# Kernel tuning notes

Measured on AMD Instinct MI355X. Metric: run time of the kernel, lower is better.

The kernel has to match this reference:

```python
import jax, jax.numpy as jnp
import numpy as np

N_EMBD = 2048
N_HEAD = 32
N_KV_HEAD = 8
HEAD_DIM = N_EMBD // N_HEAD  # 64
N_REP = N_HEAD // N_KV_HEAD  # 4
B, T = 2, 2048


def setup_inputs() -> dict:
    key = jax.random.key(0)
    ks = jax.random.split(key, 9)
    s = 1.0 / np.sqrt(N_EMBD)
    kv_dim = N_KV_HEAD * HEAD_DIM
    return {
        "x": jax.random.normal(ks[0], (B, T, N_EMBD), dtype=jnp.float32),
        "Wq": jax.random.normal(ks[1], (N_EMBD, N_EMBD), dtype=jnp.float32) * s,
        "bq": jax.random.normal(ks[2], (N_EMBD,), dtype=jnp.float32) * 0.01,
        "Wk": jax.random.normal(ks[3], (N_EMBD, kv_dim), dtype=jnp.float32) * s,
        "bk": jax.random.normal(ks[4], (kv_dim,), dtype=jnp.float32) * 0.01,
        "Wv": jax.random.normal(ks[5], (N_EMBD, kv_dim), dtype=jnp.float32) * s,
        "bv": jax.random.normal(ks[6], (kv_dim,), dtype=jnp.float32) * 0.01,
        "Wo": jax.random.normal(ks[7], (N_EMBD, N_EMBD), dtype=jnp.float32) * s,
        "bo": jax.random.normal(ks[8], (N_EMBD,), dtype=jnp.float32) * 0.01,
    }


def reference(x, Wq, bq, Wk, bk, Wv, bv, Wo, bo):
    Bsz, Tlen, C = x.shape
    # projections
    q = (x @ Wq + bq).reshape(Bsz, Tlen, N_HEAD, HEAD_DIM).transpose(0, 2, 1, 3)   # [B,H,T,d]
    k = (x @ Wk + bk).reshape(Bsz, Tlen, N_KV_HEAD, HEAD_DIM).transpose(0, 2, 1, 3)  # [B,Hkv,T,d]
    v = (x @ Wv + bv).reshape(Bsz, Tlen, N_KV_HEAD, HEAD_DIM).transpose(0, 2, 1, 3)
    # repeat_interleave KV heads to match query heads
    k = jnp.repeat(k, N_REP, axis=1)  # [B,H,T,d]
    v = jnp.repeat(v, N_REP, axis=1)
    # causal SDPA
    scale = 1.0 / jnp.sqrt(jnp.asarray(HEAD_DIM, dtype=x.dtype))
    scores = jnp.einsum('bhqd,bhkd->bhqk', q, k) * scale  # [B,H,T,T]
    causal = jnp.tril(jnp.ones((Tlen, Tlen), dtype=bool))
    scores = jnp.where(causal, scores, jnp.asarray(-jnp.inf, dtype=scores.dtype))
    attn = jax.nn.softmax(scores, axis=-1)
    y = jnp.einsum('bhqk,bhkd->bhqd', attn, v)  # [B,H,T,d]
    y = y.transpose(0, 2, 1, 3).reshape(Bsz, Tlen, C)
    return y @ Wo + bo
```

## Files before the change

### kernel.cpp

```cpp
#include <hip/hip_runtime.h>
#include <hip/hip_bf16.h>

#define B_SZ   2
#define T_SEQ  2048
#define C_EMB  2048
#define KV_DIM 512

typedef __bf16 bf16x8 __attribute__((ext_vector_type(8)));
typedef __bf16 bf16x4 __attribute__((ext_vector_type(4)));
typedef float  f32x4  __attribute__((ext_vector_type(4)));
typedef float  f32x16 __attribute__((ext_vector_type(16)));
typedef unsigned int u32;

typedef __attribute__((address_space(1))) const unsigned int gu32;
typedef __attribute__((address_space(3))) unsigned int lu32;
__device__ __forceinline__ void gload16(const void* g, void* l) {
  __builtin_amdgcn_global_load_lds((gu32*)g, (lu32*)l, 16, 0, 0);
}

__global__ __launch_bounds__(256) void cast_f32_bf16(const float* __restrict__ in,
                                                     __bf16* __restrict__ out, int n8) {
  int i = blockIdx.x * 256 + threadIdx.x;
  if (i < n8) {
    const float4* p = (const float4*)(in + (size_t)i * 8);
    float4 a = p[0], b = p[1];
    bf16x8 o;
    o[0] = (__bf16)a.x; o[1] = (__bf16)a.y; o[2] = (__bf16)a.z; o[3] = (__bf16)a.w;
    o[4] = (__bf16)b.x; o[5] = (__bf16)b.y; o[6] = (__bf16)b.z; o[7] = (__bf16)b.w;
    *(bf16x8*)(out + (size_t)i * 8) = o;
  }
}

__global__ __launch_bounds__(256) void transpose_cast_kernel(const float* __restrict__ in,
                                                             __bf16* __restrict__ out,
                                                             int R, int C) {
  __shared__ float tile[64][65];
  int c0 = blockIdx.x * 64, r0 = blockIdx.y * 64;
  int tid = threadIdx.x;
#pragma unroll
  for (int i = 0; i < 4; i++) {
    int idx = tid + i * 256;
    int row = idx >> 4;
    int c4  = (idx & 15) * 4;
    float4 v = *(const float4*)&in[(size_t)(r0 + row) * C + c0 + c4];
    tile[row][c4 + 0] = v.x; tile[row][c4 + 1] = v.y;
    tile[row][c4 + 2] = v.z; tile[row][c4 + 3] = v.w;
  }
  __syncthreads();
#pragma unroll
  for (int i = 0; i < 4; i++) {
    int idx = tid + i * 256;
    int col = idx >> 4;
    int r4  = (idx & 15) * 4;
    bf16x4 o;
    o[0] = (__bf16)tile[r4 + 0][col];
    o[1] = (__bf16)tile[r4 + 1][col];
    o[2] = (__bf16)tile[r4 + 2][col];
    o[3] = (__bf16)tile[r4 + 3][col];
    *(bf16x4*)&out[(size_t)(c0 + col) * R + r0 + r4] = o;
  }
}

__global__ __launch_bounds__(256) void concat_bias(const float* __restrict__ bq,
                                                   const float* __restrict__ bk,
                                                   const float* __restrict__ bv,
                                                   float* __restrict__ bcat) {
  int i = blockIdx.x * 256 + threadIdx.x;
  if (i < 3072) {
    float v = (i < 2048) ? bq[i] : (i < 2560 ? bk[i - 2048] : bv[i - 2560]);
    bcat[i] = v;
  }
}

template <int MODE>
__global__ __launch_bounds__(256) void gemm_bt(const __bf16* __restrict__ A,
                                               const __bf16* __restrict__ Bt,
                                               const float* __restrict__ bias,
                                               void* __restrict__ out0,
                                               __bf16* __restrict__ outK,
                                               __bf16* __restrict__ outV,
                                               int M, int N, int K) {
  __shared__ __bf16 As[128 * 32];
  __shared__ __bf16 Bs[128 * 32];
  int tid  = threadIdx.x;
  int lane = tid & 63, wave = tid >> 6;
  int wr = wave >> 1, wc = wave & 1;
  int la = lane & 15, kg = lane >> 4;
  int m0 = blockIdx.x * 128, n0 = blockIdx.y * 128;

  f32x4 acc[4][4];
#pragma unroll
  for (int i = 0; i < 4; i++)
#pragma unroll
    for (int j = 0; j < 4; j++)
#pragma unroll
      for (int r = 0; r < 4; r++) acc[i][j][r] = 0.f;

  int s0 = tid, s1 = tid + 256;
  const __bf16* ga0 = A  + (size_t)(m0 + (s0 >> 2)) * K + (s0 & 3) * 8;
  const __bf16* ga1 = A  + (size_t)(m0 + (s1 >> 2)) * K + (s1 & 3) * 8;
  const __bf16* gb0 = Bt + (size_t)(n0 + (s0 >> 2)) * K + (s0 & 3) * 8;
  const __bf16* gb1 = Bt + (size_t)(n0 + (s1 >> 2)) * K + (s1 & 3) * 8;
  __bf16* lA0 = As + (size_t)(0 * 256 + wave * 64) * 8;
  __bf16* lA1 = As + (size_t)(1 * 256 + wave * 64) * 8;
  __bf16* lB0 = Bs + (size_t)(0 * 256 + wave * 64) * 8;
  __bf16* lB1 = Bs + (size_t)(1 * 256 + wave * 64) * 8;

  for (int k0 = 0; k0 < K; k0 += 32) {
    gload16(ga0 + k0, lA0);
    gload16(ga1 + k0, lA1);
    gload16(gb0 + k0, lB0);
    gload16(gb1 + k0, lB1);
    __syncthreads();
    bf16x8 af[4], bfr[4];
#pragma unroll
    for (int i = 0; i < 4; i++) af[i]  = *(const bf16x8*)&As[(size_t)(wr * 64 + i * 16 + la) * 32 + kg * 8];
#pragma unroll
    for (int j = 0; j < 4; j++) bfr[j] = *(const bf16x8*)&Bs[(size_t)(wc * 64 + j * 16 + la) * 32 + kg * 8];
#pragma unroll
    for (int i = 0; i < 4; i++)
#pragma unroll
      for (int j = 0; j < 4; j++)
        acc[i][j] = __builtin_amdgcn_mfma_f32_16x16x32_bf16(af[i], bfr[j], acc[i][j], 0, 0, 0);
    __syncthreads();
  }

#pragma unroll
  for (int i = 0; i < 4; i++) {
    int rowb = m0 + wr * 64 + i * 16 + kg * 4;
#pragma unroll
    for (int j = 0; j < 4; j++) {
      int col = n0 + wc * 64 + j * 16 + la;
      float bv = bias[col];
#pragma unroll
      for (int r = 0; r < 4; r++) {
        float v = acc[i][j][r] + bv;
        if (MODE == 2) {
          ((float*)out0)[(size_t)(rowb + r) * N + col] = v;
        } else {
          if (n0 < 2048)      ((__bf16*)out0)[(size_t)(rowb + r) * 2048 + col] = (__bf16)v;
          else if (n0 < 2560) outK[(size_t)(rowb + r) * 512 + (col - 2048)] = (__bf16)v;
          else                outV[(size_t)(col - 2560) * M + rowb + r] = (__bf16)v;
        }
      }
    }
  }
}

__global__ __launch_bounds__(128) void attn_kernel(const __bf16* __restrict__ Q,
                                                   const __bf16* __restrict__ K,
                                                   const __bf16* __restrict__ Vt,
                                                   __bf16* __restrict__ Y) {
  __shared__ __bf16 Ylds[2][32][72];
  const int M = B_SZ * T_SEQ;
  int tid = threadIdx.x;
  int wv = tid >> 6, l = tid & 63;
  int qcol = l & 31, hh = l >> 5;
  int g = blockIdx.x;
  int w = (g & 7) * 256 + (g >> 3);
  int bh = w >> 5;
  int qt = 31 - (w & 31);
  int b = bh >> 5, hq = bh & 31, kvh = hq >> 2;
  int q0w = qt * 64 + wv * 32;

  const __bf16* qrow = Q + (size_t)(b * T_SEQ + q0w + qcol) * C_EMB + hq * 64;
  bf16x8 qf[4];
#pragma unroll
  for (int c = 0; c < 4; c++) qf[c] = *(const bf16x8*)(qrow + c * 16 + hh * 8);

  f32x16 acc0, acc1;
#pragma unroll
  for (int r = 0; r < 16; r++) { acc0[r] = 0.f; acc1[r] = 0.f; }
  float m_run = -1e30f, l_run = 0.f;
  const float SC = 0.125f * 1.44269504f;

  const __bf16* kbase = K + (size_t)(b * T_SEQ) * KV_DIM + kvh * 64;
  const __bf16* v0 = Vt + (size_t)(kvh * 64 + qcol) * M + (size_t)b * T_SEQ;
  const __bf16* v1 = v0 + (size_t)32 * M;

  for (int kb = 0; kb <= q0w; kb += 32) {
    f32x16 s;
#pragma unroll
    for (int r = 0; r < 16; r++) s[r] = 0.f;
    const __bf16* krow = kbase + (size_t)(kb + qcol) * KV_DIM;
#pragma unroll
    for (int c = 0; c < 4; c++) {
      bf16x8 kf = *(const bf16x8*)(krow + c * 16 + hh * 8);
      s = __builtin_amdgcn_mfma_f32_32x32x16_bf16(kf, qf[c], s, 0, 0, 0);
    }
    if (kb == q0w) {
#pragma unroll
      for (int r = 0; r < 16; r++) {
        int kr = (r & 3) + 8 * (r >> 2) + 4 * hh;
        s[r] = (kr <= qcol) ? s[r] : -1e30f;
      }
    }
    float mloc = s[0];
#pragma unroll
    for (int r = 1; r < 16; r++) mloc = fmaxf(mloc, s[r]);
    mloc = fmaxf(mloc, __shfl_xor(mloc, 32, 64));
    if (__any(mloc > m_run + 33.0f)) {
      float mnew = fmaxf(m_run, mloc);
      float corr = exp2f((m_run - mnew) * SC);
      l_run *= corr;
#pragma unroll
      for (int r = 0; r < 16; r++) { acc0[r] *= corr; acc1[r] *= corr; }
      m_run = mnew;
    }
    float p[16]; float ps = 0.f;
#pragma unroll
    for (int r = 0; r < 16; r++) { p[r] = exp2f((s[r] - m_run) * SC); ps += p[r]; }
    ps += __shfl_xor(ps, 32, 64);
    l_run += ps;
    u32 P[8];
#pragma unroll
    for (int j = 0; j < 8; j++) {
      union { __bf16 b2[2]; u32 u; } pk;
      pk.b2[0] = (__bf16)p[2 * j]; pk.b2[1] = (__bf16)p[2 * j + 1];
      P[j] = pk.u;
    }
    u32 xP[8];
#pragma unroll
    for (int j = 0; j < 8; j++) xP[j] = (u32)__shfl_xor((int)P[j], 32, 64);
    union { u32 u[4]; bf16x8 v; } w0u, w1u;
    w0u.u[0] = hh ? xP[2] : P[0];
    w0u.u[1] = hh ? xP[3] : P[1];
    w0u.u[2] = hh ? P[2]  : xP[0];
    w0u.u[3] = hh ? P[3]  : xP[1];
    w1u.u[0] = hh ? xP[6] : P[4];
    w1u.u[1] = hh ? xP[7] : P[5];
    w1u.u[2] = hh ? P[6]  : xP[4];
    w1u.u[3] = hh ? P[7]  : xP[5];
    const __bf16* vr0 = v0 + kb;
    const __bf16* vr1 = v1 + kb;
    bf16x8 vf00 = *(const bf16x8*)(vr0 + hh * 8);
    bf16x8 vf01 = *(const bf16x8*)(vr0 + 16 + hh * 8);
    bf16x8 vf10 = *(const bf16x8*)(vr1 + hh * 8);
    bf16x8 vf11 = *(const bf16x8*)(vr1 + 16 + hh * 8);
    acc0 = __builtin_amdgcn_mfma_f32_32x32x16_bf16(vf00, w0u.v, acc0, 0, 0, 0);
    acc0 = __builtin_amdgcn_mfma_f32_32x32x16_bf16(vf01, w1u.v, acc0, 0, 0, 0);
    acc1 = __builtin_amdgcn_mfma_f32_32x32x16_bf16(vf10, w0u.v, acc1, 0, 0, 0);
    acc1 = __builtin_amdgcn_mfma_f32_32x32x16_bf16(vf11, w1u.v, acc1, 0, 0, 0);
  }

  float inv = 1.0f / l_run;
  __bf16 (*slab)[72] = Ylds[wv];
#pragma unroll
  for (int r = 0; r < 16; r++) {
    int drow = (r & 3) + 8 * (r >> 2) + 4 * hh;
    slab[qcol][drow]      = (__bf16)(acc0[r] * inv);
    slab[qcol][32 + drow] = (__bf16)(acc1[r] * inv);
  }
  __syncthreads();
  __bf16* yrow = Y + (size_t)(b * T_SEQ + q0w + qcol) * C_EMB + hq * 64 + hh * 32;
#pragma unroll
  for (int c = 0; c < 4; c++)
    *(bf16x8*)(yrow + c * 8) = *(const bf16x8*)&slab[qcol][hh * 32 + c * 8];
}

extern "C" void kernel_launch(void* const* d_in, const int* in_sizes, int n_in,
                              void* d_out, int out_size, void* d_ws, size_t ws_size,
                              hipStream_t stream) {
  const float* x  = (const float*)d_in[0];
  const float* Wq = (const float*)d_in[1];
  const float* bq = (const float*)d_in[2];
  const float* Wk = (const float*)d_in[3];
  const float* bk = (const float*)d_in[4];
  const float* Wv = (const float*)d_in[5];
  const float* bv = (const float*)d_in[6];
  const float* Wo = (const float*)d_in[7];
  const float* bo = (const float*)d_in[8];
  float* out = (float*)d_out;

  const int M = B_SZ * T_SEQ;

  char* w = (char*)d_ws;
  __bf16* xb   = (__bf16*)w; w += (size_t)M * C_EMB * 2;
  __bf16* Wall = (__bf16*)w; w += (size_t)3072 * C_EMB * 2;
  __bf16* Wot  = (__bf16*)w; w += (size_t)C_EMB * C_EMB * 2;
  float*  bcat = (float*)w;  w += (size_t)3072 * 4;
  __bf16* qb   = (__bf16*)w; w += (size_t)M * C_EMB * 2;
  __bf16* kbf  = (__bf16*)w; w += (size_t)M * KV_DIM * 2;
  __bf16* vbt  = (__bf16*)w; w += (size_t)KV_DIM * M * 2;
  __bf16* yb   = (__bf16*)w; w += (size_t)M * C_EMB * 2;

  cast_f32_bf16<<<(M * C_EMB / 8 + 255) / 256, 256, 0, stream>>>(x, xb, M * C_EMB / 8);

  transpose_cast_kernel<<<dim3(C_EMB / 64, C_EMB / 64), 256, 0, stream>>>(Wq, Wall, C_EMB, C_EMB);
  transpose_cast_kernel<<<dim3(KV_DIM / 64, C_EMB / 64), 256, 0, stream>>>(Wk, Wall + (size_t)2048 * C_EMB, C_EMB, KV_DIM);
  transpose_cast_kernel<<<dim3(KV_DIM / 64, C_EMB / 64), 256, 0, stream>>>(Wv, Wall + (size_t)2560 * C_EMB, C_EMB, KV_DIM);
  transpose_cast_kernel<<<dim3(C_EMB / 64, C_EMB / 64), 256, 0, stream>>>(Wo, Wot, C_EMB, C_EMB);
  concat_bias<<<12, 256, 0, stream>>>(bq, bk, bv, bcat);

  gemm_bt<1><<<dim3(M / 128, 3072 / 128), 256, 0, stream>>>(xb, Wall, bcat, qb, kbf, vbt, M, 3072, C_EMB);

  attn_kernel<<<dim3(2048), 128, 0, stream>>>(qb, kbf, vbt, yb);

  gemm_bt<2><<<dim3(M / 128, C_EMB / 128), 256, 0, stream>>>(yb, Wot, bo, out, nullptr, nullptr, M, C_EMB, C_EMB);
}
```

Measured before the change: 427.0 us.

## Prefetch K tiles, fold softmax scale into Q, defer row-sum reduce in attention

The Q projection epilogue now pre-multiplies by scale·log2e, so the attention loop can use exp2 directly without per-element multiplies. The attention kernel software-pipelines K loads one tile ahead, issues V loads early, and wraps the MFMA groups in s_setprio. It also uses a tree max reduction, a lazy rescale threshold of 6 in the log2 domain, and moves the cross-half row-sum shuffle out of the loop. The block-to-tile mapping is changed to a simpler qt-major order, which may alter L2 locality for shared KV heads.

```diff
diff --git a/kernel.cpp b/kernel.cpp
--- a/kernel.cpp
+++ b/kernel.cpp
@@ -138,7 +138,7 @@
         if (MODE == 2) {
           ((float*)out0)[(size_t)(rowb + r) * N + col] = v;
         } else {
-          if (n0 < 2048)      ((__bf16*)out0)[(size_t)(rowb + r) * 2048 + col] = (__bf16)v;
+          if (n0 < 2048)      ((__bf16*)out0)[(size_t)(rowb + r) * 2048 + col] = (__bf16)(v * 0.18033688f);
           else if (n0 < 2560) outK[(size_t)(rowb + r) * 512 + (col - 2048)] = (__bf16)v;
           else                outV[(size_t)(col - 2560) * M + rowb + r] = (__bf16)v;
         }
@@ -157,9 +157,8 @@
   int wv = tid >> 6, l = tid & 63;
   int qcol = l & 31, hh = l >> 5;
   int g = blockIdx.x;
-  int w = (g & 7) * 256 + (g >> 3);
-  int bh = w >> 5;
-  int qt = 31 - (w & 31);
+  int qt = 31 - (g >> 6);
+  int bh = g & 63;
   int b = bh >> 5, hq = bh & 31, kvh = hq >> 2;
   int q0w = qt * 64 + wv * 32;
 
@@ -172,22 +171,34 @@
 #pragma unroll
   for (int r = 0; r < 16; r++) { acc0[r] = 0.f; acc1[r] = 0.f; }
   float m_run = -1e30f, l_run = 0.f;
-  const float SC = 0.125f * 1.44269504f;
-
-  const __bf16* kbase = K + (size_t)(b * T_SEQ) * KV_DIM + kvh * 64;
-  const __bf16* v0 = Vt + (size_t)(kvh * 64 + qcol) * M + (size_t)b * T_SEQ;
-  const __bf16* v1 = v0 + (size_t)32 * M;
+
+  const __bf16* kbase = K + (size_t)(b * T_SEQ + qcol) * KV_DIM + kvh * 64 + hh * 8;
+  const __bf16* vb0 = Vt + (size_t)(kvh * 64 + qcol) * M + (size_t)b * T_SEQ + hh * 8;
+  const __bf16* vb1 = vb0 + (size_t)32 * M;
+
+  bf16x8 kf[4];
+#pragma unroll
+  for (int c = 0; c < 4; c++) kf[c] = *(const bf16x8*)(kbase + c * 16);
 
   for (int kb = 0; kb <= q0w; kb += 32) {
     f32x16 s;
 #pragma unroll
     for (int r = 0; r < 16; r++) s[r] = 0.f;
-    const __bf16* krow = kbase + (size_t)(kb + qcol) * KV_DIM;
-#pragma unroll
-    for (int c = 0; c < 4; c++) {
-      bf16x8 kf = *(const bf16x8*)(krow + c * 16 + hh * 8);
-      s = __builtin_amdgcn_mfma_f32_32x32x16_bf16(kf, qf[c], s, 0, 0, 0);
-    }
+    __builtin_amdgcn_s_setprio(1);
+#pragma unroll
+    for (int c = 0; c < 4; c++)
+      s = __builtin_amdgcn_mfma_f32_32x32x16_bf16(kf[c], qf[c], s, 0, 0, 0);
+    __builtin_amdgcn_s_setprio(0);
+    {
+      int nkb = (kb + 32 <= q0w) ? kb + 32 : 0;
+      const __bf16* nk = kbase + (size_t)nkb * KV_DIM;
+#pragma unroll
+      for (int c = 0; c < 4; c++) kf[c] = *(const bf16x8*)(nk + c * 16);
+    }
+    bf16x8 vf0 = *(const bf16x8*)(vb0 + kb);
+    bf16x8 vf1 = *(const bf16x8*)(vb0 + kb + 16);
+    bf16x8 vf2 = *(const bf16x8*)(vb1 + kb);
+    bf16x8 vf3 = *(const bf16x8*)(vb1 + kb + 16);
     if (kb == q0w) {
 #pragma unroll
       for (int r = 0; r < 16; r++) {
@@ -195,28 +206,30 @@
         s[r] = (kr <= qcol) ? s[r] : -1e30f;
       }
     }
-    float mloc = s[0];
-#pragma unroll
-    for (int r = 1; r < 16; r++) mloc = fmaxf(mloc, s[r]);
+    float m01 = fmaxf(s[0], s[1]),  m23 = fmaxf(s[2], s[3]);
+    float m45 = fmaxf(s[4], s[5]),  m67 = fmaxf(s[6], s[7]);
+    float m89 = fmaxf(s[8], s[9]),  mab = fmaxf(s[10], s[11]);
+    float mcd = fmaxf(s[12], s[13]), mef = fmaxf(s[14], s[15]);
+    float mloc = fmaxf(fmaxf(fmaxf(m01, m23), fmaxf(m45, m67)),
+                       fmaxf(fmaxf(m89, mab), fmaxf(mcd, mef)));
     mloc = fmaxf(mloc, __shfl_xor(mloc, 32, 64));
-    if (__any(mloc > m_run + 33.0f)) {
+    if (__any(mloc > m_run + 6.0f)) {
       float mnew = fmaxf(m_run, mloc);
-      float corr = exp2f((m_run - mnew) * SC);
+      float corr = exp2f(m_run - mnew);
       l_run *= corr;
 #pragma unroll
       for (int r = 0; r < 16; r++) { acc0[r] *= corr; acc1[r] *= corr; }
       m_run = mnew;
     }
-    float p[16]; float ps = 0.f;
-#pragma unroll
-    for (int r = 0; r < 16; r++) { p[r] = exp2f((s[r] - m_run) * SC); ps += p[r]; }
-    ps += __shfl_xor(ps, 32, 64);
+    float ps = 0.f;
+#pragma unroll
+    for (int r = 0; r < 16; r++) { s[r] = exp2f(s[r] - m_run); ps += s[r]; }
     l_run += ps;
     u32 P[8];
 #pragma unroll
     for (int j = 0; j < 8; j++) {
       union { __bf16 b2[2]; u32 u; } pk;
-      pk.b2[0] = (__bf16)p[2 * j]; pk.b2[1] = (__bf16)p[2 * j + 1];
+      pk.b2[0] = (__bf16)s[2 * j]; pk.b2[1] = (__bf16)s[2 * j + 1];
       P[j] = pk.u;
     }
     u32 xP[8];
@@ -231,18 +244,15 @@
     w1u.u[1] = hh ? xP[7] : P[5];
     w1u.u[2] = hh ? P[6]  : xP[4];
     w1u.u[3] = hh ? P[7]  : xP[5];
-    const __bf16* vr0 = v0 + kb;
-    const __bf16* vr1 = v1 + kb;
-    bf16x8 vf00 = *(const bf16x8*)(vr0 + hh * 8);
-    bf16x8 vf01 = *(const bf16x8*)(vr0 + 16 + hh * 8);
-    bf16x8 vf10 = *(const bf16x8*)(vr1 + hh * 8);
-    bf16x8 vf11 = *(const bf16x8*)(vr1 + 16 + hh * 8);
-    acc0 = __builtin_amdgcn_mfma_f32_32x32x16_bf16(vf00, w0u.v, acc0, 0, 0, 0);
-    acc0 = __builtin_amdgcn_mfma_f32_32x32x16_bf16(vf01, w1u.v, acc0, 0, 0, 0);
-    acc1 = __builtin_amdgcn_mfma_f32_32x32x16_bf16(vf10, w0u.v, acc1, 0, 0, 0);
-    acc1 = __builtin_amdgcn_mfma_f32_32x32x16_bf16(vf11, w1u.v, acc1, 0, 0, 0);
-  }
-
+    __builtin_amdgcn_s_setprio(1);
+    acc0 = __builtin_amdgcn_mfma_f32_32x32x16_bf16(vf0, w0u.v, acc0, 0, 0, 0);
+    acc0 = __builtin_amdgcn_mfma_f32_32x32x16_bf16(vf1, w1u.v, acc0, 0, 0, 0);
+    acc1 = __builtin_amdgcn_mfma_f32_32x32x16_bf16(vf2, w0u.v, acc1, 0, 0, 0);
+    acc1 = __builtin_amdgcn_mfma_f32_32x32x16_bf16(vf3, w1u.v, acc1, 0, 0, 0);
+    __builtin_amdgcn_s_setprio(0);
+  }
+
+  l_run += __shfl_xor(l_run, 32, 64);
   float inv = 1.0f / l_run;
   __bf16 (*slab)[72] = Ylds[wv];
 #pragma unroll
```

New measurement: 382.2 us. 1.12x faster.
